# Performance work log

Measured on AMD Instinct MI355X. Metric: run time of the kernel, lower is better.

The kernel has to match this reference:

```python
import jax, jax.numpy as jnp
import numpy as np
from jax import lax

WIN = 7            # skimage default win_size
K1, K2 = 0.01, 0.03
DATA_RANGE = 1.0


def _uniform_filter_valid(x):
    # (skimage uses reflect-padded uniform_filter then crops pad=3, which equals
    #  a valid windowed mean.)
    c, h, w = x.shape
    x4 = x[:, None]                                   # (C,1,H,W)
    kh = jnp.full((1, 1, WIN, 1), 1.0 / WIN, x.dtype)
    kw = jnp.full((1, 1, 1, WIN), 1.0 / WIN, x.dtype)
    dn = ('NCHW', 'OIHW', 'NCHW')
    x4 = lax.conv_general_dilated(x4, kh, (1, 1), 'VALID', dimension_numbers=dn)
    x4 = lax.conv_general_dilated(x4, kw, (1, 1), 'VALID', dimension_numbers=dn)
    return x4[:, 0]


def setup_inputs() -> dict:
    key = jax.random.key(0)
    k1, k2 = jax.random.split(key)
    shape = (32, 3, 512, 512)
    return {
        'input_tensor': jax.random.uniform(k1, shape, dtype=jnp.float32),
        'target': jax.random.uniform(k2, shape, dtype=jnp.float32),
    }


def reference(input_tensor, target):
    h, w = input_tensor.shape[-2:]
    x = input_tensor.reshape(-1, h, w).astype(jnp.float32)
    y = target.reshape(-1, h, w).astype(jnp.float32)

    C1 = (K1 * DATA_RANGE) ** 2
    C2 = (K2 * DATA_RANGE) ** 2
    NP = WIN * WIN
    cov_norm = NP / (NP - 1.0)  # sample covariance (skimage default)

    ux = _uniform_filter_valid(x)
    uy = _uniform_filter_valid(y)
    uxx = _uniform_filter_valid(x * x)
    uyy = _uniform_filter_valid(y * y)
    uxy = _uniform_filter_valid(x * y)

    vx = cov_norm * (uxx - ux * ux)
    vy = cov_norm * (uyy - uy * uy)
    vxy = cov_norm * (uxy - ux * uy)

    S = ((2.0 * ux * uy + C1) * (2.0 * vxy + C2)) / (
        (ux * ux + uy * uy + C1) * (vx + vy + C2))
    # mean over cropped spatial map per channel, then over channels == global mean
    return jnp.mean(S)
```

## Files before the change

### kernel.cpp

```cpp
#include <hip/hip_runtime.h>


namespace {
constexpr int W      = 512;
constexpr int HH     = 512;
constexpr int NIMG   = 96;
constexpr int OW     = 506;
constexpr int RSTRIP = 23;
constexpr int NSTRIP = 22;
constexpr int SEGW   = 122;
constexpr float D1      = 0.2401f;
constexpr float D2      = 2.1609f;
constexpr float COVN    = 49.0f / 48.0f;
constexpr float COV2    = 2.0f * COVN;
constexpr float K49COV  = 49.0f * COVN;
constexpr float K49COV2 = 2.0f * 49.0f * COVN;
constexpr double NPIX   = 96.0 * 506.0 * 506.0;
}

__global__ __launch_bounds__(320, 6) void ssim_main(const float* __restrict__ X,
                                                    const float* __restrict__ Y,
                                                    double* __restrict__ acc)
{
    __shared__ float wsum[5];

    const int t    = threadIdx.x;
    const int wave = t >> 6;
    const int lane = t & 63;
    const int img  = blockIdx.y;
    const int r0   = blockIdx.x * RSTRIP;

    const int s  = wave * SEGW;
    const int lc = 2 * lane;
    int g = s + lc; if (g > W - 2) g = W - 2;

    const float* xb = X + (size_t)img * W * HH + g;
    const float* yb = Y + (size_t)img * W * HH + g;

    const bool ok0 = (lc     < SEGW) && (s + lc     < OW);
    const bool ok1 = (lc + 1 < SEGW) && (s + lc + 1 < OW);

    float V[5][2];
#pragma unroll
    for (int q = 0; q < 5; q++)
#pragma unroll
        for (int i = 0; i < 2; i++) V[q][i] = 0.0f;

#pragma unroll
    for (int k = 0; k < 6; k++) {
        float2 x2 = *(const float2*)(xb + (size_t)(r0 + k) * W);
        float2 y2 = *(const float2*)(yb + (size_t)(r0 + k) * W);
        float xs[2] = {x2.x, x2.y};
        float ys[2] = {y2.x, y2.y};
#pragma unroll
        for (int i = 0; i < 2; i++) {
            V[0][i] += xs[i];
            V[1][i] += ys[i];
            V[2][i] = fmaf(xs[i], xs[i], V[2][i]);
            V[3][i] = fmaf(ys[i], ys[i], V[3][i]);
            V[4][i] = fmaf(xs[i], ys[i], V[4][i]);
        }
    }

    float2 xn = *(const float2*)(xb + (size_t)(r0 + 6) * W);
    float2 yn = *(const float2*)(yb + (size_t)(r0 + 6) * W);

    float sacc = 0.0f;

    for (int j = 0; j < RSTRIP; j++) {
        {
            float xs[2] = {xn.x, xn.y};
            float ys[2] = {yn.x, yn.y};
#pragma unroll
            for (int i = 0; i < 2; i++) {
                V[0][i] += xs[i];
                V[1][i] += ys[i];
                V[2][i] = fmaf(xs[i], xs[i], V[2][i]);
                V[3][i] = fmaf(ys[i], ys[i], V[3][i]);
                V[4][i] = fmaf(xs[i], ys[i], V[4][i]);
            }
        }

        float2 xo  = *(const float2*)(xb + (size_t)(r0 + j) * W);
        float2 yo  = *(const float2*)(yb + (size_t)(r0 + j) * W);
        int rn = r0 + j + 7; if (rn > HH - 1) rn = HH - 1;
        float2 xn2 = *(const float2*)(xb + (size_t)rn * W);
        float2 yn2 = *(const float2*)(yb + (size_t)rn * W);

        float Hs[5][2];
#pragma unroll
        for (int q = 0; q < 5; q++) {
            float v0 = V[q][0], v1 = V[q][1];
            float P  = v0 + v1;
            float P1 = __shfl_down(P,  1);
            float P2 = __shfl_down(P,  2);
            float P3 = __shfl_down(P,  3);
            float a3 = __shfl_down(v0, 3);
            Hs[q][0] = (P  + P1) + (P2 + a3);
            Hs[q][1] = (v1 + P1) + (P2 + P3);
        }

#pragma unroll
        for (int i = 0; i < 2; i++) {
            float U0 = Hs[0][i], U1 = Hs[1][i];
            float U2 = Hs[2][i], U3 = Hs[3][i], U4 = Hs[4][i];
            float A    = U0 * U1;
            float q01  = fmaf(U0, U0, U1 * U1);
            float num1 = fmaf(2.0f, A, D1);
            float den1 = q01 + D1;
            float num2 = fmaf(K49COV2, U4, fmaf(-COV2, A, D2));
            float s23  = U2 + U3;
            float den2 = fmaf(K49COV, s23, fmaf(-COVN, q01, D2));
            float S = (num1 * num2) * __builtin_amdgcn_rcpf(den1 * den2);
            bool ok = i ? ok1 : ok0;
            sacc += ok ? S : 0.0f;
        }

        {
            float xs[2] = {xo.x, xo.y};
            float ys[2] = {yo.x, yo.y};
#pragma unroll
            for (int i = 0; i < 2; i++) {
                V[0][i] -= xs[i];
                V[1][i] -= ys[i];
                V[2][i] = fmaf(-xs[i], xs[i], V[2][i]);
                V[3][i] = fmaf(-ys[i], ys[i], V[3][i]);
                V[4][i] = fmaf(-xs[i], ys[i], V[4][i]);
            }
        }
        xn = xn2; yn = yn2;
    }

#pragma unroll
    for (int off = 32; off > 0; off >>= 1)
        sacc += __shfl_down(sacc, off);
    if (lane == 0) wsum[wave] = sacc;
    __syncthreads();
    if (t == 0) {
        float b = ((wsum[0] + wsum[1]) + (wsum[2] + wsum[3])) + wsum[4];
        atomicAdd(acc, (double)b);
    }
}

__global__ void ssim_finalize(const double* __restrict__ acc, float* __restrict__ out)
{
    out[0] = (float)(acc[0] / NPIX);
}

extern "C" void kernel_launch(void* const* d_in, const int* in_sizes, int n_in,
                              void* d_out, int out_size, void* d_ws, size_t ws_size,
                              hipStream_t stream)
{
    const float* X = (const float*)d_in[0];
    const float* Y = (const float*)d_in[1];
    float* out = (float*)d_out;
    double* acc = (double*)d_ws;

    hipMemsetAsync(d_ws, 0, sizeof(double), stream);
    ssim_main<<<dim3(NSTRIP, NIMG), 320, 0, stream>>>(X, Y, acc);
    ssim_finalize<<<1, 1, 0, stream>>>(acc, out);
}
```

Baseline: 243.6 us.

## Compute eight columns per lane with running horizontal sums in single-wave blocks

Each lane now owns eight contiguous columns loaded with float4 loads, and the horizontal 7-tap sum is computed as a sliding update using a shift-by-one shuffle from the neighbouring lane. Blocks shrink to one wave and the LDS/syncthreads reduction is replaced by a direct per-wave atomic. This cuts shuffles and arithmetic per output pixel, but it reduces the total number of resident waves fivefold and raises register pressure, which may hurt latency hiding.

Measured after the change: 253.1 us. 1.04x slower.

```diff
diff --git a/kernel.cpp b/kernel.cpp
--- a/kernel.cpp
+++ b/kernel.cpp
@@ -8,7 +8,6 @@
 constexpr int OW     = 506;
 constexpr int RSTRIP = 23;
 constexpr int NSTRIP = 22;
-constexpr int SEGW   = 122;
 constexpr float D1      = 0.2401f;
 constexpr float D2      = 2.1609f;
 constexpr float COVN    = 49.0f / 48.0f;
@@ -18,92 +17,84 @@
 constexpr double NPIX   = 96.0 * 506.0 * 506.0;
 }
 
-__global__ __launch_bounds__(320, 6) void ssim_main(const float* __restrict__ X,
-                                                    const float* __restrict__ Y,
-                                                    double* __restrict__ acc)
+__global__ __launch_bounds__(64, 3) void ssim_main(const float* __restrict__ X,
+                                                   const float* __restrict__ Y,
+                                                   double* __restrict__ acc)
 {
-    __shared__ float wsum[5];
-
-    const int t    = threadIdx.x;
-    const int wave = t >> 6;
-    const int lane = t & 63;
+    const int lane = threadIdx.x;
     const int img  = blockIdx.y;
     const int r0   = blockIdx.x * RSTRIP;
+    const int c0   = lane * 8;
 
-    const int s  = wave * SEGW;
-    const int lc = 2 * lane;
-    int g = s + lc; if (g > W - 2) g = W - 2;
+    const float* xb = X + (size_t)img * (W * HH) + c0;
+    const float* yb = Y + (size_t)img * (W * HH) + c0;
 
-    const float* xb = X + (size_t)img * W * HH + g;
-    const float* yb = Y + (size_t)img * W * HH + g;
-
-    const bool ok0 = (lc     < SEGW) && (s + lc     < OW);
-    const bool ok1 = (lc + 1 < SEGW) && (s + lc + 1 < OW);
-
-    float V[5][2];
+    float V[5][8];
 #pragma unroll
     for (int q = 0; q < 5; q++)
 #pragma unroll
-        for (int i = 0; i < 2; i++) V[q][i] = 0.0f;
+        for (int i = 0; i < 8; i++) V[q][i] = 0.0f;
+
+    float xr[8], yr[8], xo[8], yo[8];
+
+    auto load_row = [&](int r, float (&dx)[8], float (&dy)[8]) {
+        const float* px = xb + (size_t)r * W;
+        const float* py = yb + (size_t)r * W;
+        float4 a = *(const float4*)px;
+        float4 b = *(const float4*)(px + 4);
+        dx[0] = a.x; dx[1] = a.y; dx[2] = a.z; dx[3] = a.w;
+        dx[4] = b.x; dx[5] = b.y; dx[6] = b.z; dx[7] = b.w;
+        float4 e = *(const float4*)py;
+        float4 f = *(const float4*)(py + 4);
+        dy[0] = e.x; dy[1] = e.y; dy[2] = e.z; dy[3] = e.w;
+        dy[4] = f.x; dy[5] = f.y; dy[6] = f.z; dy[7] = f.w;
+    };
 
 #pragma unroll
     for (int k = 0; k < 6; k++) {
-        float2 x2 = *(const float2*)(xb + (size_t)(r0 + k) * W);
-        float2 y2 = *(const float2*)(yb + (size_t)(r0 + k) * W);
-        float xs[2] = {x2.x, x2.y};
-        float ys[2] = {y2.x, y2.y};
+        load_row(r0 + k, xr, yr);
 #pragma unroll
-        for (int i = 0; i < 2; i++) {
-            V[0][i] += xs[i];
-            V[1][i] += ys[i];
-            V[2][i] = fmaf(xs[i], xs[i], V[2][i]);
-            V[3][i] = fmaf(ys[i], ys[i], V[3][i]);
-            V[4][i] = fmaf(xs[i], ys[i], V[4][i]);
+        for (int i = 0; i < 8; i++) {
+            V[0][i] += xr[i];
+            V[1][i] += yr[i];
+            V[2][i] = fmaf(xr[i], xr[i], V[2][i]);
+            V[3][i] = fmaf(yr[i], yr[i], V[3][i]);
+            V[4][i] = fmaf(xr[i], yr[i], V[4][i]);
         }
     }
-
-    float2 xn = *(const float2*)(xb + (size_t)(r0 + 6) * W);
-    float2 yn = *(const float2*)(yb + (size_t)(r0 + 6) * W);
+    load_row(r0 + 6, xr, yr);
 
     float sacc = 0.0f;
 
     for (int j = 0; j < RSTRIP; j++) {
-        {
-            float xs[2] = {xn.x, xn.y};
-            float ys[2] = {yn.x, yn.y};
 #pragma unroll
-            for (int i = 0; i < 2; i++) {
-                V[0][i] += xs[i];
-                V[1][i] += ys[i];
-                V[2][i] = fmaf(xs[i], xs[i], V[2][i]);
-                V[3][i] = fmaf(ys[i], ys[i], V[3][i]);
-                V[4][i] = fmaf(xs[i], ys[i], V[4][i]);
-            }
+        for (int i = 0; i < 8; i++) {
+            V[0][i] += xr[i];
+            V[1][i] += yr[i];
+            V[2][i] = fmaf(xr[i], xr[i], V[2][i]);
+            V[3][i] = fmaf(yr[i], yr[i], V[3][i]);
+            V[4][i] = fmaf(xr[i], yr[i], V[4][i]);
         }
 
-        float2 xo  = *(const float2*)(xb + (size_t)(r0 + j) * W);
-        float2 yo  = *(const float2*)(yb + (size_t)(r0 + j) * W);
+        load_row(r0 + j, xo, yo);
         int rn = r0 + j + 7; if (rn > HH - 1) rn = HH - 1;
-        float2 xn2 = *(const float2*)(xb + (size_t)rn * W);
-        float2 yn2 = *(const float2*)(yb + (size_t)rn * W);
+        load_row(rn, xr, yr);
 
-        float Hs[5][2];
+        float Vh[5][6];
 #pragma unroll
-        for (int q = 0; q < 5; q++) {
-            float v0 = V[q][0], v1 = V[q][1];
-            float P  = v0 + v1;
-            float P1 = __shfl_down(P,  1);
-            float P2 = __shfl_down(P,  2);
-            float P3 = __shfl_down(P,  3);
-            float a3 = __shfl_down(v0, 3);
-            Hs[q][0] = (P  + P1) + (P2 + a3);
-            Hs[q][1] = (v1 + P1) + (P2 + P3);
-        }
+        for (int q = 0; q < 5; q++)
+#pragma unroll
+            for (int i = 0; i < 6; i++) Vh[q][i] = __shfl_down(V[q][i], 1);
+
+        float H[5];
+#pragma unroll
+        for (int q = 0; q < 5; q++)
+            H[q] = ((V[q][0] + V[q][1]) + (V[q][2] + V[q][3])) +
+                   ((V[q][4] + V[q][5]) + V[q][6]);
 
 #pragma unroll
-        for (int i = 0; i < 2; i++) {
-            float U0 = Hs[0][i], U1 = Hs[1][i];
-            float U2 = Hs[2][i], U3 = Hs[3][i], U4 = Hs[4][i];
+        for (int i = 0; i < 8; i++) {
+            float U0 = H[0], U1 = H[1], U2 = H[2], U3 = H[3], U4 = H[4];
             float A    = U0 * U1;
             float q01  = fmaf(U0, U0, U1 * U1);
             float num1 = fmaf(2.0f, A, D1);
@@ -112,34 +103,30 @@
             float s23  = U2 + U3;
             float den2 = fmaf(K49COV, s23, fmaf(-COVN, q01, D2));
             float S = (num1 * num2) * __builtin_amdgcn_rcpf(den1 * den2);
-            bool ok = i ? ok1 : ok0;
-            sacc += ok ? S : 0.0f;
+            sacc += (c0 + i < OW) ? S : 0.0f;
+            if (i < 7) {
+#pragma unroll
+                for (int q = 0; q < 5; q++) {
+                    float addv = (i == 0) ? V[q][7] : Vh[q][i - 1];
+                    H[q] += addv - V[q][i];
+                }
+            }
         }
 
-        {
-            float xs[2] = {xo.x, xo.y};
-            float ys[2] = {yo.x, yo.y};
 #pragma unroll
-            for (int i = 0; i < 2; i++) {
-                V[0][i] -= xs[i];
-                V[1][i] -= ys[i];
-                V[2][i] = fmaf(-xs[i], xs[i], V[2][i]);
-                V[3][i] = fmaf(-ys[i], ys[i], V[3][i]);
-                V[4][i] = fmaf(-xs[i], ys[i], V[4][i]);
-            }
+        for (int i = 0; i < 8; i++) {
+            V[0][i] -= xo[i];
+            V[1][i] -= yo[i];
+            V[2][i] = fmaf(-xo[i], xo[i], V[2][i]);
+            V[3][i] = fmaf(-yo[i], yo[i], V[3][i]);
+            V[4][i] = fmaf(-xo[i], yo[i], V[4][i]);
         }
-        xn = xn2; yn = yn2;
     }
 
 #pragma unroll
     for (int off = 32; off > 0; off >>= 1)
         sacc += __shfl_down(sacc, off);
-    if (lane == 0) wsum[wave] = sacc;
-    __syncthreads();
-    if (t == 0) {
-        float b = ((wsum[0] + wsum[1]) + (wsum[2] + wsum[3])) + wsum[4];
-        atomicAdd(acc, (double)b);
-    }
+    if (lane == 0) atomicAdd(acc, (double)sacc);
 }
 
 __global__ void ssim_finalize(const double* __restrict__ acc, float* __restrict__ out)
@@ -157,6 +144,6 @@
     double* acc = (double*)d_ws;
 
     hipMemsetAsync(d_ws, 0, sizeof(double), stream);
-    ssim_main<<<dim3(NSTRIP, NIMG), 320, 0, stream>>>(X, Y, acc);
+    ssim_main<<<dim3(NSTRIP, NIMG), 64, 0, stream>>>(X, Y, acc);
     ssim_finalize<<<1, 1, 0, stream>>>(acc, out);
 }
```
